# Performance work log

Measured on AMD Instinct MI355X. Metric: run time of the kernel, lower is better.

The kernel has to match this reference:

```python
import jax, jax.numpy as jnp
import numpy as np

B, N, CIN, COUT = 2, 150000, 64, 64
SPATIAL = (128, 128, 128)  # spatial_shape forward arg, fixed here (list arg)
EPS = 1e-5


def setup_inputs() -> dict:
    key = jax.random.key(0)
    k1, k2, k3 = jax.random.split(key, 3)
    features = jax.random.normal(k1, (B, N, CIN), jnp.float32)
    coordinates = jax.random.randint(k2, (B, N, 3), 0, SPATIAL[0], jnp.int32)
    # SparseConv3d weight: 3x3x3 kernel flattened to 27 offsets, [27, Cin, Cout]
    weight = jax.random.normal(k3, (27, CIN, COUT), jnp.float32) * 0.05
    gamma = jnp.ones((COUT,), jnp.float32)
    beta = jnp.zeros((COUT,), jnp.float32)
    return {"features": features, "coordinates": coordinates, "weight": weight,
            "gamma": gamma, "beta": beta, "batch_size": B}


def _rulebook_ids(coordinates, batch_size):
    """For each of 27 kernel offsets, the flat input-point id feeding each output
    site (output sites = input sites, rulebook gather). Empty/OOB -> BN (zero row)."""
    X, Y, Z = SPATIAL
    Np = coordinates.shape[1]
    BN = batch_size * Np
    pid = jnp.arange(BN, dtype=jnp.int32)
    b = jnp.repeat(jnp.arange(batch_size, dtype=jnp.int32), Np)
    c = coordinates.reshape(-1, 3)
    # dense voxel hash: coord -> point id (max for deterministic collision handling)
    grid = jnp.full((batch_size, X, Y, Z), -1, jnp.int32)
    grid = grid.at[b, c[:, 0], c[:, 1], c[:, 2]].max(pid)
    # 27 offsets in {-1,0,1}^3 (padding=1, kernel=3, stride=1)
    r = jnp.arange(-1, 2, dtype=jnp.int32)
    offs = jnp.stack(jnp.meshgrid(r, r, r, indexing="ij"), -1).reshape(27, 3)
    nc = c[None, :, :] + offs[:, None, :]                      # [27, BN, 3]
    hi = jnp.array([X, Y, Z], jnp.int32)
    valid = jnp.all((nc >= 0) & (nc < hi), axis=-1)            # [27, BN]
    ncc = jnp.clip(nc, 0, hi - 1)
    ids = grid[b[None, :], ncc[..., 0], ncc[..., 1], ncc[..., 2]]
    return jnp.where(valid & (ids >= 0), ids, BN)              # BN -> zero row


def reference(features, coordinates, weight, gamma, beta, batch_size):
    Bs, Np, Cin = features.shape
    BN = Bs * Np
    ids = _rulebook_ids(coordinates, batch_size)               # [27, BN]
    feats = jnp.concatenate(
        [features.reshape(BN, Cin), jnp.zeros((1, Cin), features.dtype)], 0)

    # gather-GEMM-scatter accumulated over the 27 kernel offsets
    def step(acc, xs):
        idk, wk = xs
        return acc + feats[idk] @ wk, None

    out0 = jnp.zeros((BN, weight.shape[-1]), features.dtype)
    out, _ = jax.lax.scan(step, out0, (ids, weight))

    # BatchNorm1d (training stats over all points) + ReLU
    mean = out.mean(axis=0)
    var = out.var(axis=0)
    out = (out - mean) * jax.lax.rsqrt(var + EPS) * gamma + beta
    out = jax.nn.relu(out)
    return out.reshape(Bs, Np, -1)
```

## Files before the change

kernel.cpp:

```cpp
#include <hip/hip_runtime.h>

#define GS 128
#define GS3 (GS*GS*GS)
#define NPTS 150000
#define NBATCH 2
#define BN_TOT (NBATCH*NPTS)
#define CONV_BLOCKS 1172
#define BN_PAD (CONV_BLOCKS*256)
#define ZROW   BN_PAD
#define EPS 1e-5f
#define NBKT 8192

#define OFF_GRID   0ull
#define SZ_GRID    ((size_t)NBATCH*GS3*4)
#define OFF_WFRAG  (OFF_GRID + SZ_GRID)
#define SZ_WFRAG   ((size_t)27*4096*2)
#define OFF_STATS  (OFF_WFRAG + SZ_WFRAG)
#define OFF_CNT    (OFF_STATS + 512)
#define OFF_CUR    (OFF_CNT + NBKT*4)
#define OFF_SIDX   (OFF_CUR + NBKT*4)
#define OFF_CSORT  (OFF_SIDX + 1200128)
#define OFF_FB16S  (OFF_CSORT + (size_t)BN_PAD*16)

typedef __attribute__((ext_vector_type(8))) short bf16x8;
typedef __attribute__((ext_vector_type(4))) float f32x4;
typedef unsigned int u32;
typedef const __attribute__((address_space(1))) u32* gas_u32p;
typedef __attribute__((address_space(3))) u32* las_u32p;

__device__ __forceinline__ short f2bf(float f) {
    union { float f; unsigned u; } v; v.f = f;
    unsigned rr = v.u + 0x7fffu + ((v.u >> 16) & 1u);
    return (short)(rr >> 16);
}

__global__ __launch_bounds__(256) void k_count(const int* __restrict__ coords,
                                               int* __restrict__ grid,
                                               u32* __restrict__ cnt) {
    int p = blockIdx.x*256 + threadIdx.x;
    if (p >= BN_TOT) return;
    int x = coords[p*3+0], y = coords[p*3+1], z = coords[p*3+2];
    int b = (p >= NPTS);
    atomicMax(&grid[(b<<21) | (x<<14) | (y<<7) | z], p);
    atomicAdd(&cnt[(b<<12) | ((x>>3)<<8) | ((y>>3)<<4) | (z>>3)], 1u);
}

__global__ __launch_bounds__(1024) void k_scan(const u32* __restrict__ cnt,
                                               u32* __restrict__ cur) {
    __shared__ u32 ps[1024];
    int t = threadIdx.x;
    u32 l[8]; u32 s = 0;
    #pragma unroll
    for (int i = 0; i < 8; ++i) { l[i] = cnt[t*8+i]; s += l[i]; }
    ps[t] = s; __syncthreads();
    for (int off = 1; off < 1024; off <<= 1) {
        u32 v = (t >= off) ? ps[t-off] : 0u; __syncthreads();
        ps[t] += v; __syncthreads();
    }
    u32 run = (t == 0) ? 0u : ps[t-1];
    #pragma unroll
    for (int i = 0; i < 8; ++i) { cur[t*8+i] = run; run += l[i]; }
}

__global__ __launch_bounds__(256) void k_place(const float* __restrict__ feats,
                                               const int* __restrict__ coords,
                                               u32* __restrict__ cur,
                                               int* __restrict__ sortidx,
                                               int4* __restrict__ csorted,
                                               ushort* __restrict__ fb16s) {
    int p = blockIdx.x*256 + threadIdx.x;
    if (p >= BN_PAD) return;
    if (p >= BN_TOT) { csorted[p] = make_int4(-9,-9,-9,0); return; }
    int x = coords[p*3+0], y = coords[p*3+1], z = coords[p*3+2];
    int b = (p >= NPTS);
    int bkt = (b<<12) | ((x>>3)<<8) | ((y>>3)<<4) | (z>>3);
    int pos = (int)atomicAdd(&cur[bkt], 1u);
    sortidx[p] = pos;
    csorted[pos] = make_int4(x, y, z, p);
    const float4* s = (const float4*)(feats + (size_t)p*64);
    ushort* d = fb16s + (size_t)pos*64;
    #pragma unroll
    for (int i = 0; i < 8; ++i) {
        float4 a = s[2*i], c = s[2*i+1];
        ushort4 u0 = { (ushort)f2bf(a.x),(ushort)f2bf(a.y),(ushort)f2bf(a.z),(ushort)f2bf(a.w) };
        ushort4 u1 = { (ushort)f2bf(c.x),(ushort)f2bf(c.y),(ushort)f2bf(c.z),(ushort)f2bf(c.w) };
        ((ushort4*)d)[2*i] = u0; ((ushort4*)d)[2*i+1] = u1;
    }
}

__global__ __launch_bounds__(256) void k_prefrag(const float* __restrict__ w,
                                                 short* __restrict__ wfrag) {
    int t = blockIdx.x * 256 + threadIdx.x;
    if (t >= 27*4096) return;
    int i    = t & 7;
    int lane = (t >> 3) & 63;
    int tt   = (t >> 9) & 3;
    int c    = (t >> 11) & 1;
    int k    = t >> 12;
    int kk = c*32 + (lane >> 4)*8 + i;
    int co = tt*16 + (lane & 15);
    wfrag[t] = f2bf(w[(k*64 + kk)*64 + co]);
}

__global__ __launch_bounds__(256, 2) void k_conv(
    const ushort* __restrict__ fb16s,
    const int4* __restrict__ csorted,
    const int* __restrict__ grid,
    const int* __restrict__ sortidx,
    const ushort* __restrict__ wfrag,
    float* __restrict__ out,
    float* __restrict__ gstats)
{
    __shared__ __align__(16) ushort bufs[2][4096];
    __shared__ int ids_lds[27*256];
    __shared__ float bsum[64], bsq[64];

    const int tid  = threadIdx.x;
    const int lane = tid & 63;
    const int wv   = tid >> 6;
    const int r    = lane & 15;
    const int seg  = lane >> 4;
    const int p0b  = blockIdx.x * 256;
    const int rbase = wv*64 + r;

    {
        int4 c = csorted[p0b + tid];
        const bool pad = (p0b + tid >= BN_TOT);
        const int gb = (c.w >= NPTS) ? GS3 : 0;
        #pragma unroll
        for (int k = 0; k < 27; ++k) {
            int dx = k/9 - 1, dy = (k/3)%3 - 1, dz = k%3 - 1;
            int nx = c.x+dx, ny = c.y+dy, nz = c.z+dz;
            int ok = (int)(!pad & ((unsigned)nx < 128u) & ((unsigned)ny < 128u) &
                           ((unsigned)nz < 128u));
            int pid = grid[gb + ((nx&127)<<14) + ((ny&127)<<7) + (nz&127)];
            pid = ok ? pid : -1;
            int sv = sortidx[pid < 0 ? 0 : pid];
            ids_lds[k*256 + tid] = (pid >= 0) ? sv : ZROW;
        }
    }
    if (tid < 64) { bsum[tid] = 0.f; bsq[tid] = 0.f; }
    __syncthreads();

    auto stage = [&](int kk, int bsel) {
        #pragma unroll
        for (int c = 0; c < 2; ++c) {
            int chunk = c*4 + wv;
            const u32* g = (const u32*)(wfrag + (size_t)kk*4096 + chunk*512) + lane*4;
            u32* l = (u32*)(&bufs[bsel][chunk*512]);
            __builtin_amdgcn_global_load_lds((gas_u32p)g, (las_u32p)l, 16, 0, 0);
        }
    };

#define LDA16(AC, S) { _Pragma("unroll") for (int t_ = 0; t_ < 4; ++t_) {     \
        const ushort* ap_ = fb16s + (size_t)(S)[t_]*64 + seg*8;               \
        AC[2*t_]   = *(const bf16x8*)(ap_);                                   \
        AC[2*t_+1] = *(const bf16x8*)(ap_ + 32); } }
#define LDIDS(S, kk) { _Pragma("unroll") for (int t_ = 0; t_ < 4; ++t_)       \
        S[t_] = ids_lds[(kk)*256 + rbase + t_*16]; }

    f32x4 acc[4][4];
    #pragma unroll
    for (int t = 0; t < 4; ++t)
        #pragma unroll
        for (int q = 0; q < 4; ++q) acc[t][q] = (f32x4){0,0,0,0};

    bf16x8 aE[8], aO[8];
    int sE[4], sO[4];

    LDIDS(sE, 0); LDIDS(sO, 1);
    __builtin_amdgcn_sched_barrier(0);
    LDA16(aE, sE);
    __builtin_amdgcn_sched_barrier(0);
    stage(0, 0);
    __builtin_amdgcn_sched_barrier(0);
    LDA16(aO, sO);
    __builtin_amdgcn_sched_barrier(0);

    auto phase = [&](int k, bf16x8 (&AC)[8]) {
        asm volatile("s_waitcnt vmcnt(8)" ::: "memory");
        __builtin_amdgcn_sched_barrier(0);
        __builtin_amdgcn_s_barrier();
        __builtin_amdgcn_sched_barrier(0);
        const ushort* bb = bufs[k & 1];
        bf16x8 b0 = *(const bf16x8*)(bb + 0*512 + lane*8);
        bf16x8 b1 = *(const bf16x8*)(bb + 1*512 + lane*8);
        bf16x8 b2 = *(const bf16x8*)(bb + 2*512 + lane*8);
        bf16x8 b3 = *(const bf16x8*)(bb + 3*512 + lane*8);
        bf16x8 b4 = *(const bf16x8*)(bb + 4*512 + lane*8);
        bf16x8 b5 = *(const bf16x8*)(bb + 5*512 + lane*8);
        bf16x8 b6 = *(const bf16x8*)(bb + 6*512 + lane*8);
        bf16x8 b7 = *(const bf16x8*)(bb + 7*512 + lane*8);
        int kp2 = (k+2 > 26) ? 26 : k+2;
        int sn[4]; LDIDS(sn, kp2);
        if (k < 26) stage(k+1, (k+1) & 1);
        __builtin_amdgcn_sched_barrier(0);
        __builtin_amdgcn_s_setprio(1);
        #pragma unroll
        for (int t = 0; t < 4; ++t) {
            acc[t][0] = __builtin_amdgcn_mfma_f32_16x16x32_bf16(AC[2*t], b0, acc[t][0], 0,0,0);
            acc[t][1] = __builtin_amdgcn_mfma_f32_16x16x32_bf16(AC[2*t], b1, acc[t][1], 0,0,0);
            acc[t][2] = __builtin_amdgcn_mfma_f32_16x16x32_bf16(AC[2*t], b2, acc[t][2], 0,0,0);
            acc[t][3] = __builtin_amdgcn_mfma_f32_16x16x32_bf16(AC[2*t], b3, acc[t][3], 0,0,0);
            acc[t][0] = __builtin_amdgcn_mfma_f32_16x16x32_bf16(AC[2*t+1], b4, acc[t][0], 0,0,0);
            acc[t][1] = __builtin_amdgcn_mfma_f32_16x16x32_bf16(AC[2*t+1], b5, acc[t][1], 0,0,0);
            acc[t][2] = __builtin_amdgcn_mfma_f32_16x16x32_bf16(AC[2*t+1], b6, acc[t][2], 0,0,0);
            acc[t][3] = __builtin_amdgcn_mfma_f32_16x16x32_bf16(AC[2*t+1], b7, acc[t][3], 0,0,0);
        }
        __builtin_amdgcn_s_setprio(0);
        __builtin_amdgcn_sched_barrier(0);
        LDA16(AC, sn);
        __builtin_amdgcn_sched_barrier(0);
    };

    #pragma unroll 1
    for (int t = 0; t < 13; ++t) {
        phase(2*t,   aE);
        phase(2*t+1, aO);
    }
    phase(26, aE);

    #pragma unroll
    for (int t = 0; t < 4; ++t) {
        #pragma unroll
        for (int j = 0; j < 4; ++j) {
            int row = p0b + wv*64 + t*16 + seg*4 + j;
            if (row < BN_TOT) {
                int opid = csorted[row].w;
                float* ob = out + (size_t)opid*64 + r;
                ob[ 0] = acc[t][0][j];
                ob[16] = acc[t][1][j];
                ob[32] = acc[t][2][j];
                ob[48] = acc[t][3][j];
            }
        }
    }

    float s_[4] = {0,0,0,0}, q_[4] = {0,0,0,0};
    #pragma unroll
    for (int q = 0; q < 4; ++q)
        #pragma unroll
        for (int t = 0; t < 4; ++t)
            #pragma unroll
            for (int j = 0; j < 4; ++j) {
                float v = acc[t][q][j]; s_[q] += v; q_[q] += v*v;
            }
    #pragma unroll
    for (int q = 0; q < 4; ++q) {
        atomicAdd(&bsum[q*16 + r], s_[q]);
        atomicAdd(&bsq [q*16 + r], q_[q]);
    }
    __syncthreads();
    if (tid < 64) { atomicAdd(&gstats[tid], bsum[tid]); atomicAdd(&gstats[64+tid], bsq[tid]); }
#undef LDA16
#undef LDIDS
}

__global__ __launch_bounds__(256) void k_norm(float* __restrict__ out,
                                              const float* __restrict__ stats,
                                              const float* __restrict__ gamma,
                                              const float* __restrict__ beta) {
    int i = blockIdx.x*256 + threadIdx.x;
    const int n4 = BN_TOT*16;
    if (i >= n4) return;
    float4 v = ((const float4*)out)[i];
    int ch = (i & 15) * 4;
    float o[4] = {v.x, v.y, v.z, v.w};
    float rp[4];
    #pragma unroll
    for (int j = 0; j < 4; ++j) {
        int c = ch + j;
        float mean = stats[c] * (1.f/BN_TOT);
        float var  = stats[64+c] * (1.f/BN_TOT) - mean*mean;
        float y = (o[j] - mean) * rsqrtf(var + EPS) * gamma[c] + beta[c];
        rp[j] = fmaxf(y, 0.f);
    }
    float4 rv; rv.x = rp[0]; rv.y = rp[1]; rv.z = rp[2]; rv.w = rp[3];
    ((float4*)out)[i] = rv;
}

extern "C" void kernel_launch(void* const* d_in, const int* in_sizes, int n_in,
                              void* d_out, int out_size, void* d_ws, size_t ws_size,
                              hipStream_t stream) {
    const float* feats  = (const float*)d_in[0];
    const int*   coords = (const int*)d_in[1];
    const float* weight = (const float*)d_in[2];
    const float* gamma  = (const float*)d_in[3];
    const float* beta   = (const float*)d_in[4];
    float* out = (float*)d_out;

    char*   ws      = (char*)d_ws;
    int*    grid    = (int*)(ws + OFF_GRID);
    short*  wfrag   = (short*)(ws + OFF_WFRAG);
    float*  stats   = (float*)(ws + OFF_STATS);
    u32*    cnt     = (u32*)(ws + OFF_CNT);
    u32*    cur     = (u32*)(ws + OFF_CUR);
    int*    sortidx = (int*)(ws + OFF_SIDX);
    int4*   csorted = (int4*)(ws + OFF_CSORT);
    ushort* fb16s   = (ushort*)(ws + OFF_FB16S);

    hipMemsetAsync(grid,  0xFF, SZ_GRID, stream);
    hipMemsetAsync(stats, 0, 512, stream);
    hipMemsetAsync(cnt,   0, NBKT*4, stream);
    hipMemsetAsync(fb16s + (size_t)BN_TOT*64, 0,
                   (size_t)(BN_PAD + 1 - BN_TOT)*128, stream);

    k_count  <<<(BN_TOT + 255)/256, 256, 0, stream>>>(coords, grid, cnt);
    k_scan   <<<1, 1024, 0, stream>>>(cnt, cur);
    k_place  <<<(BN_PAD + 255)/256, 256, 0, stream>>>(feats, coords, cur,
                                                      sortidx, csorted, fb16s);
    k_prefrag<<<(27*4096)/256, 256, 0, stream>>>(weight, wfrag);
    k_conv   <<<CONV_BLOCKS, 256, 0, stream>>>(fb16s, csorted, grid, sortidx,
                                               (const ushort*)wfrag, out, stats);
    k_norm   <<<(BN_TOT*16)/256, 256, 0, stream>>>(out, stats, gamma, beta);
}
```

Before: 227.0 us.

## Load weight fragments directly into registers instead of LDS double-buffering

Removes the LDS double buffer and the global_load_lds staging of weight fragments. Each wave now loads its B fragments straight from global memory (L2/L1-cached) into registers, two offsets ahead, alongside the A gathers. This drops the per-offset workgroup barrier and the LDS reads. In exchange it uses more VGPRs for the extra B registers, and the launch-bounds occupancy hint of 2 is removed. Every wave also issues redundant global weight loads.

```diff
diff --git a/kernel.cpp b/kernel.cpp
--- a/kernel.cpp
+++ b/kernel.cpp
@@ -25,8 +25,6 @@
 typedef __attribute__((ext_vector_type(8))) short bf16x8;
 typedef __attribute__((ext_vector_type(4))) float f32x4;
 typedef unsigned int u32;
-typedef const __attribute__((address_space(1))) u32* gas_u32p;
-typedef __attribute__((address_space(3))) u32* las_u32p;
 
 __device__ __forceinline__ short f2bf(float f) {
     union { float f; unsigned u; } v; v.f = f;
@@ -102,7 +100,7 @@
     wfrag[t] = f2bf(w[(k*64 + kk)*64 + co]);
 }
 
-__global__ __launch_bounds__(256, 2) void k_conv(
+__global__ __launch_bounds__(256) void k_conv(
     const ushort* __restrict__ fb16s,
     const int4* __restrict__ csorted,
     const int* __restrict__ grid,
@@ -111,7 +109,6 @@
     float* __restrict__ out,
     float* __restrict__ gstats)
 {
-    __shared__ __align__(16) ushort bufs[2][4096];
     __shared__ int ids_lds[27*256];
     __shared__ float bsum[64], bsq[64];
 
@@ -142,20 +139,12 @@
     if (tid < 64) { bsum[tid] = 0.f; bsq[tid] = 0.f; }
     __syncthreads();
 
-    auto stage = [&](int kk, int bsel) {
-        #pragma unroll
-        for (int c = 0; c < 2; ++c) {
-            int chunk = c*4 + wv;
-            const u32* g = (const u32*)(wfrag + (size_t)kk*4096 + chunk*512) + lane*4;
-            u32* l = (u32*)(&bufs[bsel][chunk*512]);
-            __builtin_amdgcn_global_load_lds((gas_u32p)g, (las_u32p)l, 16, 0, 0);
-        }
-    };
-
 #define LDA16(AC, S) { _Pragma("unroll") for (int t_ = 0; t_ < 4; ++t_) {     \
         const ushort* ap_ = fb16s + (size_t)(S)[t_]*64 + seg*8;               \
         AC[2*t_]   = *(const bf16x8*)(ap_);                                   \
         AC[2*t_+1] = *(const bf16x8*)(ap_ + 32); } }
+#define LDB8(BC, kk) { const bf16x8* wp_ = (const bf16x8*)wfrag + (size_t)(kk)*512; \
+        _Pragma("unroll") for (int f_ = 0; f_ < 8; ++f_) BC[f_] = wp_[f_*64 + lane]; }
 #define LDIDS(S, kk) { _Pragma("unroll") for (int t_ = 0; t_ < 4; ++t_)       \
         S[t_] = ids_lds[(kk)*256 + rbase + t_*16]; }
 
@@ -165,60 +154,48 @@
         #pragma unroll
         for (int q = 0; q < 4; ++q) acc[t][q] = (f32x4){0,0,0,0};
 
-    bf16x8 aE[8], aO[8];
+    bf16x8 aE[8], aO[8], bE[8], bO[8];
     int sE[4], sO[4];
 
     LDIDS(sE, 0); LDIDS(sO, 1);
     __builtin_amdgcn_sched_barrier(0);
+    LDB8(bE, 0);
     LDA16(aE, sE);
     __builtin_amdgcn_sched_barrier(0);
-    stage(0, 0);
-    __builtin_amdgcn_sched_barrier(0);
+    LDB8(bO, 1);
     LDA16(aO, sO);
     __builtin_amdgcn_sched_barrier(0);
 
-    auto phase = [&](int k, bf16x8 (&AC)[8]) {
-        asm volatile("s_waitcnt vmcnt(8)" ::: "memory");
-        __builtin_amdgcn_sched_barrier(0);
-        __builtin_amdgcn_s_barrier();
-        __builtin_amdgcn_sched_barrier(0);
-        const ushort* bb = bufs[k & 1];
-        bf16x8 b0 = *(const bf16x8*)(bb + 0*512 + lane*8);
-        bf16x8 b1 = *(const bf16x8*)(bb + 1*512 + lane*8);
-        bf16x8 b2 = *(const bf16x8*)(bb + 2*512 + lane*8);
-        bf16x8 b3 = *(const bf16x8*)(bb + 3*512 + lane*8);
-        bf16x8 b4 = *(const bf16x8*)(bb + 4*512 + lane*8);
-        bf16x8 b5 = *(const bf16x8*)(bb + 5*512 + lane*8);
-        bf16x8 b6 = *(const bf16x8*)(bb + 6*512 + lane*8);
-        bf16x8 b7 = *(const bf16x8*)(bb + 7*512 + lane*8);
+    auto phase = [&](int k, bf16x8 (&AC)[8], bf16x8 (&BC)[8]) {
         int kp2 = (k+2 > 26) ? 26 : k+2;
         int sn[4]; LDIDS(sn, kp2);
-        if (k < 26) stage(k+1, (k+1) & 1);
+        asm volatile("s_waitcnt vmcnt(16)" ::: "memory");
         __builtin_amdgcn_sched_barrier(0);
         __builtin_amdgcn_s_setprio(1);
         #pragma unroll
         for (int t = 0; t < 4; ++t) {
-            acc[t][0] = __builtin_amdgcn_mfma_f32_16x16x32_bf16(AC[2*t], b0, acc[t][0], 0,0,0);
-            acc[t][1] = __builtin_amdgcn_mfma_f32_16x16x32_bf16(AC[2*t], b1, acc[t][1], 0,0,0);
-            acc[t][2] = __builtin_amdgcn_mfma_f32_16x16x32_bf16(AC[2*t], b2, acc[t][2], 0,0,0);
-            acc[t][3] = __builtin_amdgcn_mfma_f32_16x16x32_bf16(AC[2*t], b3, acc[t][3], 0,0,0);
-            acc[t][0] = __builtin_amdgcn_mfma_f32_16x16x32_bf16(AC[2*t+1], b4, acc[t][0], 0,0,0);
-            acc[t][1] = __builtin_amdgcn_mfma_f32_16x16x32_bf16(AC[2*t+1], b5, acc[t][1], 0,0,0);
-            acc[t][2] = __builtin_amdgcn_mfma_f32_16x16x32_bf16(AC[2*t+1], b6, acc[t][2], 0,0,0);
-            acc[t][3] = __builtin_amdgcn_mfma_f32_16x16x32_bf16(AC[2*t+1], b7, acc[t][3], 0,0,0);
+            acc[t][0] = __builtin_amdgcn_mfma_f32_16x16x32_bf16(AC[2*t], BC[0], acc[t][0], 0,0,0);
+            acc[t][1] = __builtin_amdgcn_mfma_f32_16x16x32_bf16(AC[2*t], BC[1], acc[t][1], 0,0,0);
+            acc[t][2] = __builtin_amdgcn_mfma_f32_16x16x32_bf16(AC[2*t], BC[2], acc[t][2], 0,0,0);
+            acc[t][3] = __builtin_amdgcn_mfma_f32_16x16x32_bf16(AC[2*t], BC[3], acc[t][3], 0,0,0);
+            acc[t][0] = __builtin_amdgcn_mfma_f32_16x16x32_bf16(AC[2*t+1], BC[4], acc[t][0], 0,0,0);
+            acc[t][1] = __builtin_amdgcn_mfma_f32_16x16x32_bf16(AC[2*t+1], BC[5], acc[t][1], 0,0,0);
+            acc[t][2] = __builtin_amdgcn_mfma_f32_16x16x32_bf16(AC[2*t+1], BC[6], acc[t][2], 0,0,0);
+            acc[t][3] = __builtin_amdgcn_mfma_f32_16x16x32_bf16(AC[2*t+1], BC[7], acc[t][3], 0,0,0);
         }
         __builtin_amdgcn_s_setprio(0);
         __builtin_amdgcn_sched_barrier(0);
+        LDB8(BC, kp2);
         LDA16(AC, sn);
         __builtin_amdgcn_sched_barrier(0);
     };
 
     #pragma unroll 1
     for (int t = 0; t < 13; ++t) {
-        phase(2*t,   aE);
-        phase(2*t+1, aO);
-    }
-    phase(26, aE);
+        phase(2*t,   aE, bE);
+        phase(2*t+1, aO, bO);
+    }
+    phase(26, aE, bE);
 
     #pragma unroll
     for (int t = 0; t < 4; ++t) {
@@ -253,6 +230,7 @@
     __syncthreads();
     if (tid < 64) { atomicAdd(&gstats[tid], bsum[tid]); atomicAdd(&gstats[64+tid], bsq[tid]); }
 #undef LDA16
+#undef LDB8
 #undef LDIDS
 }
 
```

Result: slower. 248.3 us (+9.4%).

## Switch conv GEMM from 16x16x32 to 32x32x16 bf16 MFMA tiles

Applied to the files above, without the earlier changes.

Replaces the 16x16x32 MFMA tiling (4 row tiles by 4 column tiles per wave) with 32x32x16 MFMAs (2 row tiles by 2 column tiles). The weight pre-fragmentation, gathered-row loading, output scatter and BN statistics reduction are all rewritten to match the new fragment layout. This cuts the MFMA instruction count and the number of gathered rows each lane loads per offset, and widens the contiguous output write per lane. It also drops the min-2-blocks occupancy hint from launch_bounds, so register pressure and occupancy may shift.

```diff
diff --git a/kernel.cpp b/kernel.cpp
--- a/kernel.cpp
+++ b/kernel.cpp
@@ -22,8 +22,8 @@
 #define OFF_CSORT  (OFF_SIDX + 1200128)
 #define OFF_FB16S  (OFF_CSORT + (size_t)BN_PAD*16)
 
-typedef __attribute__((ext_vector_type(8))) short bf16x8;
-typedef __attribute__((ext_vector_type(4))) float f32x4;
+typedef __attribute__((ext_vector_type(8)))  short bf16x8;
+typedef __attribute__((ext_vector_type(16))) float f32x16;
 typedef unsigned int u32;
 typedef const __attribute__((address_space(1))) u32* gas_u32p;
 typedef __attribute__((address_space(3))) u32* las_u32p;
@@ -94,15 +94,15 @@
     if (t >= 27*4096) return;
     int i    = t & 7;
     int lane = (t >> 3) & 63;
-    int tt   = (t >> 9) & 3;
-    int c    = (t >> 11) & 1;
+    int kt   = (t >> 9) & 3;
+    int ct   = (t >> 11) & 1;
     int k    = t >> 12;
-    int kk = c*32 + (lane >> 4)*8 + i;
-    int co = tt*16 + (lane & 15);
+    int kk = kt*16 + (lane >> 5)*8 + i;
+    int co = ct*32 + (lane & 31);
     wfrag[t] = f2bf(w[(k*64 + kk)*64 + co]);
 }
 
-__global__ __launch_bounds__(256, 2) void k_conv(
+__global__ __launch_bounds__(256) void k_conv(
     const ushort* __restrict__ fb16s,
     const int4* __restrict__ csorted,
     const int* __restrict__ grid,
@@ -118,10 +118,10 @@
     const int tid  = threadIdx.x;
     const int lane = tid & 63;
     const int wv   = tid >> 6;
-    const int r    = lane & 15;
-    const int seg  = lane >> 4;
+    const int l31  = lane & 31;
+    const int lh   = lane >> 5;
     const int p0b  = blockIdx.x * 256;
-    const int rbase = wv*64 + r;
+    const int rb32 = wv*64 + l31;
 
     {
         int4 c = csorted[p0b + tid];
@@ -152,29 +152,31 @@
         }
     };
 
-#define LDA16(AC, S) { _Pragma("unroll") for (int t_ = 0; t_ < 4; ++t_) {     \
-        const ushort* ap_ = fb16s + (size_t)(S)[t_]*64 + seg*8;               \
-        AC[2*t_]   = *(const bf16x8*)(ap_);                                   \
-        AC[2*t_+1] = *(const bf16x8*)(ap_ + 32); } }
-#define LDIDS(S, kk) { _Pragma("unroll") for (int t_ = 0; t_ < 4; ++t_)       \
-        S[t_] = ids_lds[(kk)*256 + rbase + t_*16]; }
-
-    f32x4 acc[4][4];
-    #pragma unroll
-    for (int t = 0; t < 4; ++t)
-        #pragma unroll
-        for (int q = 0; q < 4; ++q) acc[t][q] = (f32x4){0,0,0,0};
+#define LDA8(AC, S) { _Pragma("unroll") for (int rt_ = 0; rt_ < 2; ++rt_) {   \
+        const ushort* ap_ = fb16s + (size_t)(S)[rt_]*64 + lh*8;               \
+        AC[rt_*4+0] = *(const bf16x8*)(ap_);                                  \
+        AC[rt_*4+1] = *(const bf16x8*)(ap_ + 16);                             \
+        AC[rt_*4+2] = *(const bf16x8*)(ap_ + 32);                             \
+        AC[rt_*4+3] = *(const bf16x8*)(ap_ + 48); } }
+#define LDIDS(S, kk) { S[0] = ids_lds[(kk)*256 + rb32];                       \
+                       S[1] = ids_lds[(kk)*256 + rb32 + 32]; }
+
+    f32x16 acc[2][2];
+    #pragma unroll
+    for (int rt = 0; rt < 2; ++rt)
+        #pragma unroll
+        for (int ct = 0; ct < 2; ++ct) acc[rt][ct] = (f32x16)(0.f);
 
     bf16x8 aE[8], aO[8];
-    int sE[4], sO[4];
+    int sE[2], sO[2];
 
     LDIDS(sE, 0); LDIDS(sO, 1);
     __builtin_amdgcn_sched_barrier(0);
-    LDA16(aE, sE);
+    LDA8(aE, sE);
     __builtin_amdgcn_sched_barrier(0);
     stage(0, 0);
     __builtin_amdgcn_sched_barrier(0);
-    LDA16(aO, sO);
+    LDA8(aO, sO);
     __builtin_amdgcn_sched_barrier(0);
 
     auto phase = [&](int k, bf16x8 (&AC)[8]) {
@@ -183,33 +185,25 @@
         __builtin_amdgcn_s_barrier();
         __builtin_amdgcn_sched_barrier(0);
         const ushort* bb = bufs[k & 1];
-        bf16x8 b0 = *(const bf16x8*)(bb + 0*512 + lane*8);
-        bf16x8 b1 = *(const bf16x8*)(bb + 1*512 + lane*8);
-        bf16x8 b2 = *(const bf16x8*)(bb + 2*512 + lane*8);
-        bf16x8 b3 = *(const bf16x8*)(bb + 3*512 + lane*8);
-        bf16x8 b4 = *(const bf16x8*)(bb + 4*512 + lane*8);
-        bf16x8 b5 = *(const bf16x8*)(bb + 5*512 + lane*8);
-        bf16x8 b6 = *(const bf16x8*)(bb + 6*512 + lane*8);
-        bf16x8 b7 = *(const bf16x8*)(bb + 7*512 + lane*8);
+        bf16x8 B[8];
+        #pragma unroll
+        for (int f = 0; f < 8; ++f)
+            B[f] = *(const bf16x8*)(bb + f*512 + lane*8);
         int kp2 = (k+2 > 26) ? 26 : k+2;
-        int sn[4]; LDIDS(sn, kp2);
+        int sn[2]; LDIDS(sn, kp2);
         if (k < 26) stage(k+1, (k+1) & 1);
         __builtin_amdgcn_sched_barrier(0);
         __builtin_amdgcn_s_setprio(1);
         #pragma unroll
-        for (int t = 0; t < 4; ++t) {
-            acc[t][0] = __builtin_amdgcn_mfma_f32_16x16x32_bf16(AC[2*t], b0, acc[t][0], 0,0,0);
-            acc[t][1] = __builtin_amdgcn_mfma_f32_16x16x32_bf16(AC[2*t], b1, acc[t][1], 0,0,0);
-            acc[t][2] = __builtin_amdgcn_mfma_f32_16x16x32_bf16(AC[2*t], b2, acc[t][2], 0,0,0);
-            acc[t][3] = __builtin_amdgcn_mfma_f32_16x16x32_bf16(AC[2*t], b3, acc[t][3], 0,0,0);
-            acc[t][0] = __builtin_amdgcn_mfma_f32_16x16x32_bf16(AC[2*t+1], b4, acc[t][0], 0,0,0);
-            acc[t][1] = __builtin_amdgcn_mfma_f32_16x16x32_bf16(AC[2*t+1], b5, acc[t][1], 0,0,0);
-            acc[t][2] = __builtin_amdgcn_mfma_f32_16x16x32_bf16(AC[2*t+1], b6, acc[t][2], 0,0,0);
-            acc[t][3] = __builtin_amdgcn_mfma_f32_16x16x32_bf16(AC[2*t+1], b7, acc[t][3], 0,0,0);
+        for (int kt = 0; kt < 4; ++kt) {
+            acc[0][0] = __builtin_amdgcn_mfma_f32_32x32x16_bf16(AC[kt],   B[kt],   acc[0][0], 0,0,0);
+            acc[0][1] = __builtin_amdgcn_mfma_f32_32x32x16_bf16(AC[kt],   B[4+kt], acc[0][1], 0,0,0);
+            acc[1][0] = __builtin_amdgcn_mfma_f32_32x32x16_bf16(AC[4+kt], B[kt],   acc[1][0], 0,0,0);
+            acc[1][1] = __builtin_amdgcn_mfma_f32_32x32x16_bf16(AC[4+kt], B[4+kt], acc[1][1], 0,0,0);
         }
         __builtin_amdgcn_s_setprio(0);
         __builtin_amdgcn_sched_barrier(0);
-        LDA16(AC, sn);
+        LDA8(AC, sn);
         __builtin_amdgcn_sched_barrier(0);
     };
 
@@ -221,38 +215,35 @@
     phase(26, aE);
 
     #pragma unroll
-    for (int t = 0; t < 4; ++t) {
-        #pragma unroll
-        for (int j = 0; j < 4; ++j) {
-            int row = p0b + wv*64 + t*16 + seg*4 + j;
-            if (row < BN_TOT) {
-                int opid = csorted[row].w;
-                float* ob = out + (size_t)opid*64 + r;
-                ob[ 0] = acc[t][0][j];
-                ob[16] = acc[t][1][j];
-                ob[32] = acc[t][2][j];
-                ob[48] = acc[t][3][j];
+    for (int rt = 0; rt < 2; ++rt) {
+        #pragma unroll
+        for (int g = 0; g < 4; ++g) {
+            #pragma unroll
+            for (int q = 0; q < 4; ++q) {
+                int row = p0b + wv*64 + rt*32 + q + 8*g + 4*lh;
+                if (row < BN_TOT) {
+                    int opid = csorted[row].w;
+                    float* ob = out + (size_t)opid*64 + l31;
+                    ob[ 0] = acc[rt][0][g*4+q];
+                    ob[32] = acc[rt][1][g*4+q];
+                }
             }
         }
     }
 
-    float s_[4] = {0,0,0,0}, q_[4] = {0,0,0,0};
-    #pragma unroll
-    for (int q = 0; q < 4; ++q)
-        #pragma unroll
-        for (int t = 0; t < 4; ++t)
-            #pragma unroll
-            for (int j = 0; j < 4; ++j) {
-                float v = acc[t][q][j]; s_[q] += v; q_[q] += v*v;
-            }
-    #pragma unroll
-    for (int q = 0; q < 4; ++q) {
-        atomicAdd(&bsum[q*16 + r], s_[q]);
-        atomicAdd(&bsq [q*16 + r], q_[q]);
-    }
+    float s0 = 0.f, q0 = 0.f, s1 = 0.f, q1 = 0.f;
+    #pragma unroll
+    for (int rt = 0; rt < 2; ++rt)
+        #pragma unroll
+        for (int e = 0; e < 16; ++e) {
+            float v0 = acc[rt][0][e]; s0 += v0; q0 += v0*v0;
+            float v1 = acc[rt][1][e]; s1 += v1; q1 += v1*v1;
+        }
+    atomicAdd(&bsum[l31],      s0);  atomicAdd(&bsq[l31],      q0);
+    atomicAdd(&bsum[32 + l31], s1);  atomicAdd(&bsq[32 + l31], q1);
     __syncthreads();
     if (tid < 64) { atomicAdd(&gstats[tid], bsum[tid]); atomicAdd(&gstats[64+tid], bsq[tid]); }
-#undef LDA16
+#undef LDA8
 #undef LDIDS
 }
 
```

Measured after the change: 235.7 us. 3.9% more time.
